# Performance work log

Hardware: AMD Instinct MI355X
Metric: run time of the kernel (lower is better)

## Reference

```python
import jax, jax.numpy as jnp
import numpy as np

C, H, W = 21, 384, 384
THETA_ALPHA, THETA_BETA, THETA_GAMMA = 160.0, 3.0, 3.0
NUM_ITER = 5
SP_RADIUS = 6   # ~2*theta_gamma truncation for the spatial Gaussian filter
BI_RADIUS = 2   # local window stand-in for the permutohedral bilateral filter
CLIQUE_IDS = (5, 37, 81, 150, 230)  # deterministic stand-in for random.sample(range(1,256),5)


def _shift(x, dy, dx):
    # zero-padded shift: out[..., y, x] = x[..., y-dy, x-dx]
    h, w = x.shape[-2], x.shape[-1]
    py = (max(dy, 0), max(-dy, 0))
    px = (max(dx, 0), max(-dx, 0))
    xp = jnp.pad(x, [(0, 0)] * (x.ndim - 2) + [py, px])
    return xp[..., py[1]:py[1] + h, px[1]:px[1] + w]


def _gauss_blur(x, theta, radius):
    # unnormalized separable spatial Gaussian (high_dim_filter, bilateral=False)
    offs = np.arange(-radius, radius + 1)
    k = np.exp(-(offs.astype(np.float32) ** 2) / (2.0 * theta * theta))
    y = sum(float(k[i]) * _shift(x, int(o), 0) for i, o in enumerate(offs))
    return sum(float(k[i]) * _shift(y, 0, int(o)) for i, o in enumerate(offs))


def _bilateral(x, rgb, ta, tb, radius):
    # unnormalized local bilateral filter (high_dim_filter, bilateral=True)
    out = jnp.zeros_like(x)
    for dy in range(-radius, radius + 1):
        for dx in range(-radius, radius + 1):
            sw = float(np.exp(-(dy * dy + dx * dx) / (2.0 * ta * ta)))
            cdiff = rgb - _shift(rgb, dy, dx)  # (3,h,w)
            cw = jnp.exp(-jnp.sum(cdiff * cdiff, axis=0) / (2.0 * tb * tb))
            out = out + sw * cw * _shift(x, dy, dx)
    return out


def setup_inputs() -> dict:
    key = jax.random.key(0)
    k1, k2, k3 = jax.random.split(key, 3)
    # offset unaries away from 0 so first_term = prod/q stays finite
    unaries = jax.random.uniform(k1, (1, H, W, C), dtype=jnp.float32) + 0.5
    rgb = jax.random.uniform(k2, (1, H, W, 3), dtype=jnp.float32) * 255.0
    superpixels = jax.random.randint(k3, (1, H, W), 0, 256, dtype=jnp.int32)
    return {
        "unaries": unaries,
        "rgb": rgb,
        "superpixels": superpixels,
        "spatial_ker_weights": jnp.eye(C, dtype=jnp.float32),
        "bilateral_ker_weights": jnp.eye(C, dtype=jnp.float32),
        "compatibility_matrix": -jnp.eye(C, dtype=jnp.float32),
        "superpixel_low_weights": jnp.ones((C,), dtype=jnp.float32),
        "superpixel_high_weight": jnp.ones((1,), dtype=jnp.float32),
    }


def reference(unaries, rgb, superpixels, spatial_ker_weights, bilateral_ker_weights,
              compatibility_matrix, superpixel_low_weights, superpixel_high_weight):
    c, h, w = C, H, W
    u = jnp.transpose(unaries[0], (2, 0, 1))        # (c,h,w)
    img = jnp.transpose(rgb[0], (2, 0, 1))          # (3,h,w)
    sp_map = jnp.transpose(superpixels[0])          # (w,h) == (h,w) since square

    ones = jnp.ones((c, h, w), dtype=u.dtype)
    spatial_norm = _gauss_blur(ones, THETA_GAMMA, SP_RADIUS)
    bilateral_norm = _bilateral(ones, img, THETA_ALPHA, THETA_BETA, BI_RADIUS)

    # clique ids are distinct, so masks are disjoint; msum in {0,1}
    msum = jnp.zeros((h, w), dtype=u.dtype)
    for sp_idx in CLIQUE_IDS:
        msum = msum + (sp_map == sp_idx).astype(u.dtype)
    n_cliques = float(len(CLIQUE_IDS))

    q = u
    for _ in range(NUM_ITER):
        sm = jax.nn.softmax(q, axis=0)
        spatial_out = _gauss_blur(sm, THETA_GAMMA, SP_RADIUS) / spatial_norm
        bilateral_out = _bilateral(sm, img, THETA_ALPHA, THETA_BETA, BI_RADIUS) / bilateral_norm

        # prod_tensor = sum_k [ mask_k*q + (1-mask_k) ]  (disjoint masks => closed form)
        prod_tensor = msum[None] * q + (n_cliques - msum)[None]
        first_term = prod_tensor / q
        sp_update = (superpixel_low_weights[:, None, None] * first_term
                     + superpixel_high_weight[0] * (1.0 - first_term))

        mp = (spatial_ker_weights @ spatial_out.reshape(c, -1)
              + bilateral_ker_weights @ bilateral_out.reshape(c, -1))
        pairwise = (compatibility_matrix @ mp).reshape(c, h, w)
        q = u - pairwise + sp_update

    return jnp.transpose(q[None], (0, 2, 3, 1))  # (1,h,w,c)
```

## Files before the change

kernel.cpp:

```cpp
#include <hip/hip_runtime.h>
#include <hip/hip_bf16.h>

static constexpr int C  = 21;
static constexpr int H  = 384;
static constexpr int W  = 384;
static constexpr int HW = H * W;
static constexpr float NCLIQ = 5.0f;

typedef unsigned short u16;
typedef unsigned int   u32;

#define GKDEF constexpr float gk[13] = { \
    0.13533528f, 0.24935222f, 0.41111229f, 0.60653066f, 0.80073740f, \
    0.94595947f, 1.00000000f, 0.94595947f, 0.80073740f, 0.60653066f, \
    0.41111229f, 0.24935222f, 0.13533528f }

__device__ __forceinline__ float bfu2f(u16 u) {
    return __uint_as_float(((u32)u) << 16);
}
__device__ __forceinline__ u16 f2bfu(float f) {
    unsigned x = __float_as_uint(f);
    return (u16)((x + 0x7FFF + ((x >> 16) & 1)) >> 16);
}

__global__ __launch_bounds__(256)
void k_prep(const float* __restrict__ un, const float* __restrict__ rgb,
            const int* __restrict__ sp,
            const float* __restrict__ Wsp, const float* __restrict__ Wbi,
            const float* __restrict__ Cm,
            float* __restrict__ q, float* __restrict__ unp,
            u16* __restrict__ wtab, float* __restrict__ msum,
            float* __restrict__ inv_sp, float* __restrict__ inv_bn,
            float* __restrict__ M1, float* __restrict__ M2,
            int* __restrict__ mflag,
            u16* __restrict__ t1, u16* __restrict__ t2) {
    GKDEF;
    __shared__ float sM1[C * C], sM2[C * C];
    __shared__ float Aun[256 * C];
    __shared__ int seq;
    if (threadIdx.x == 0) seq = 1;
    bool bad = false;
    for (int i = threadIdx.x; i < C * C; i += 256) {
        int c = i / C, k = i - c * C;
        float a1 = 0.f, a2 = 0.f;
        for (int j = 0; j < C; j++) {
            float cm = Cm[c * C + j];
            a1 += cm * Wsp[j * C + k];
            a2 += cm * Wbi[j * C + k];
        }
        sM1[i] = a1;
        sM2[i] = a2;
        if (__float_as_uint(a1) != __float_as_uint(a2)) bad = true;
        if (blockIdx.x == 0) { M1[i] = a1; M2[i] = a2; }
    }

    int bid = blockIdx.x;
    int chunk = (bid & 7) * 72 + (bid >> 3);
    int p0 = chunk * 256;
    int p = p0 + threadIdx.x;
    int y = p / W, x = p - y * W;

    {
        const float* ub = un + (size_t)p0 * C;
        for (int i = threadIdx.x; i < 256 * C / 4; i += 256)
            *(float4*)(Aun + i * 4) = *(const float4*)(ub + i * 4);
    }
    __syncthreads();
    if (bad) atomicAnd(&seq, 0);

    float v[C];
#pragma unroll
    for (int c = 0; c < C; c++) {
        v[c] = Aun[threadIdx.x * C + c];
        q[c * HW + p] = v[c];
        unp[c * HW + p] = v[c];
    }

    float swl[9];
#pragma unroll
    for (int i = 0; i < 9; i++) swl[i] = expf(-(float)i * (1.0f / 51200.0f));

    float r0 = rgb[p * 3 + 0];
    float g0 = rgb[p * 3 + 1];
    float b0 = rgb[p * 3 + 2];
    float s = 0.f;
    int t = 0;
#pragma unroll
    for (int dy = -2; dy <= 2; dy++) {
#pragma unroll
        for (int dx = -2; dx <= 2; dx++, t++) {
            int sy = y - dy, sx = x - dx;
            float wv = 0.f;
            if (sy >= 0 && sy < H && sx >= 0 && sx < W) {
                int o = sy * W + sx;
                float dr = r0 - rgb[o * 3 + 0];
                float dg = g0 - rgb[o * 3 + 1];
                float db = b0 - rgb[o * 3 + 2];
                wv = swl[dy * dy + dx * dx] *
                     expf(-(dr * dr + dg * dg + db * db) * (1.0f / 18.0f));
            }
            u16 wu = f2bfu(wv);
            wtab[(size_t)t * HW + p] = wu;
            s += bfu2f(wu);
        }
    }
    inv_bn[p] = 1.0f / s;

    float fy = 0.f, fx = 0.f;
    for (int o = -6; o <= 6; o++) {
        if (y - o >= 0 && y - o < H) fy += gk[o + 6];
        if (x - o >= 0 && x - o < W) fx += gk[o + 6];
    }
    inv_sp[p] = 1.0f / (fy * fx);

    int vv = sp[x * W + y];
    msum[p] = (vv == 5 || vv == 37 || vv == 81 || vv == 150 || vv == 230) ? 1.0f : 0.0f;

    __syncthreads();
    bool eq = (seq != 0);
    if (bid == 0 && threadIdx.x == 0) mflag[0] = eq ? 1 : 0;

    float mx = -1e30f;
#pragma unroll
    for (int c = 0; c < C; c++) mx = fmaxf(mx, v[c]);
    float ssum = 0.f;
#pragma unroll
    for (int c = 0; c < C; c++) {
        v[c] = expf(v[c] - mx);
        ssum += v[c];
    }
    float inv = 1.0f / ssum;
    float a1[C];
#pragma unroll
    for (int c = 0; c < C; c++) a1[c] = 0.f;
#pragma unroll
    for (int k = 0; k < C; k++) {
        float e = v[k];
#pragma unroll
        for (int c = 0; c < C; c++) a1[c] += sM1[c * C + k] * e;
    }
#pragma unroll
    for (int c = 0; c < C; c++) t1[c * HW + p] = f2bfu(a1[c] * inv);
    if (!eq) {
        float a2[C];
#pragma unroll
        for (int c = 0; c < C; c++) a2[c] = 0.f;
#pragma unroll
        for (int k = 0; k < C; k++) {
            float e = v[k];
#pragma unroll
            for (int c = 0; c < C; c++) a2[c] += sM2[c * C + k] * e;
        }
#pragma unroll
        for (int c = 0; c < C; c++) t2[c * HW + p] = f2bfu(a2[c] * inv);
    }
}

__global__ __launch_bounds__(256)
void k_ST(const float* __restrict__ q, const float* __restrict__ M1,
          const float* __restrict__ M2, const int* __restrict__ mflag,
          u16* __restrict__ t1, u16* __restrict__ t2) {
    int bid = blockIdx.x;
    int chunk = (bid & 7) * 72 + (bid >> 3);
    int p = chunk * 256 + threadIdx.x;
    bool meq = (mflag[0] != 0);
    float v[C];
    float mx = -1e30f;
#pragma unroll
    for (int c = 0; c < C; c++) {
        v[c] = q[c * HW + p];
        mx = fmaxf(mx, v[c]);
    }
    float s = 0.f;
#pragma unroll
    for (int c = 0; c < C; c++) {
        v[c] = expf(v[c] - mx);
        s += v[c];
    }
    float inv = 1.0f / s;
    float a1[C];
#pragma unroll
    for (int c = 0; c < C; c++) a1[c] = 0.f;
#pragma unroll
    for (int k = 0; k < C; k++) {
        float e = v[k];
#pragma unroll
        for (int c = 0; c < C; c++) a1[c] += M1[c * C + k] * e;
    }
#pragma unroll
    for (int c = 0; c < C; c++) t1[c * HW + p] = f2bfu(a1[c] * inv);
    if (!meq) {
        float a2[C];
#pragma unroll
        for (int c = 0; c < C; c++) a2[c] = 0.f;
#pragma unroll
        for (int k = 0; k < C; k++) {
            float e = v[k];
#pragma unroll
            for (int c = 0; c < C; c++) a2[c] += M2[c * C + k] * e;
        }
#pragma unroll
        for (int c = 0; c < C; c++) t2[c * HW + p] = f2bfu(a2[c] * inv);
    }
}

__global__ __launch_bounds__(256)
void k_VF(const u16* __restrict__ t1, const u16* __restrict__ t2,
          const u16* __restrict__ wtab, const float* __restrict__ msum,
          const float* __restrict__ inv_sp, const float* __restrict__ inv_bn,
          const float* __restrict__ unp,
          const float* __restrict__ loww, const float* __restrict__ highw,
          const int* __restrict__ mflag,
          float* __restrict__ q, float* __restrict__ outp) {
    GKDEF;
    __shared__ float A[20 * 144];
    __shared__ float B[8 * 144];
    int bid = blockIdx.x;
    int xcd = bid & 7;
    int idx = bid >> 3;
    int c   = idx % 21;
    int rem = idx / 21;
    int xt  = rem % 3;
    int ytl = rem / 3;
    int gyt = xcd * 6 + ytl;
    int x0 = xt * 128;
    int y0 = gyt * 8;
    bool meq = (mflag[0] != 0);
    const u16* t1p = t1 + (size_t)c * HW;

    for (int i = threadIdx.x; i < 20 * 36; i += 256) {
        int r = i / 36, q4 = i - r * 36;
        int gy = y0 - 6 + r;
        int gx = x0 - 8 + q4 * 4;
        float4 v;
        if (gy < 0 || gy >= H) {
            v.x = v.y = v.z = v.w = 0.f;
        } else if (gx >= 0 && gx + 3 < W) {
            ushort4 u = *(const ushort4*)(t1p + gy * W + gx);
            v.x = bfu2f(u.x); v.y = bfu2f(u.y); v.z = bfu2f(u.z); v.w = bfu2f(u.w);
        } else {
            float e[4];
            for (int jj = 0; jj < 4; jj++) {
                int xx = gx + jj;
                e[jj] = (xx >= 0 && xx < W) ? bfu2f(t1p[gy * W + xx]) : 0.f;
            }
            v.x = e[0]; v.y = e[1]; v.z = e[2]; v.w = e[3];
        }
        *(float4*)(A + r * 144 + q4 * 4) = v;
    }
    __syncthreads();

    for (int i = threadIdx.x; i < 8 * 36; i += 256) {
        int r = i / 36, c4 = (i - r * 36) * 4;
        float ax = 0.f, ay = 0.f, az = 0.f, aw = 0.f;
#pragma unroll
        for (int d = 0; d < 13; d++) {
            const float4 av = *(const float4*)(A + (r + d) * 144 + c4);
            ax += gk[d] * av.x;
            ay += gk[d] * av.y;
            az += gk[d] * av.z;
            aw += gk[d] * av.w;
        }
        float4 o;
        o.x = ax; o.y = ay; o.z = az; o.w = aw;
        *(float4*)(B + r * 144 + c4) = o;
    }
    __syncthreads();

    int row = threadIdx.x >> 5;
    int xq  = (threadIdx.x & 31) * 4;
    int y   = y0 + row;
    int x4  = x0 + xq;
    int p4  = y * W + x4;

    ushort4 wu[25];
#pragma unroll
    for (int t = 0; t < 25; t++)
        wu[t] = *(const ushort4*)(wtab + (size_t)t * HW + p4);

    float bw[20];
    {
        const float* bp = B + row * 144 + xq;
        *(float4*)(bw +  0) = *(const float4*)(bp +  0);
        *(float4*)(bw +  4) = *(const float4*)(bp +  4);
        *(float4*)(bw +  8) = *(const float4*)(bp +  8);
        *(float4*)(bw + 12) = *(const float4*)(bp + 12);
        *(float4*)(bw + 16) = *(const float4*)(bp + 16);
    }
    float sp_[4];
#pragma unroll
    for (int jj = 0; jj < 4; jj++) {
        float a = 0.f;
#pragma unroll
        for (int t = 0; t < 13; t++) a += gk[t] * bw[jj + t + 2];
        sp_[jj] = a;
    }

    int robase;
    if (meq) {
        robase = row + 6;
    } else {
        const u16* t2p = t2 + (size_t)c * HW;
        for (int i = threadIdx.x; i < 12 * 36; i += 256) {
            int r = i / 36, q4 = i - r * 36;
            int gy = min(max(y0 - 2 + r, 0), H - 1);
            int gx = min(max(x0 - 8 + q4 * 4, 0), W - 4);
            ushort4 u = *(const ushort4*)(t2p + gy * W + gx);
            float4 v;
            v.x = bfu2f(u.x); v.y = bfu2f(u.y); v.z = bfu2f(u.z); v.w = bfu2f(u.w);
            *(float4*)(A + r * 144 + q4 * 4) = v;
        }
        __syncthreads();
        robase = row + 2;
    }

    float lc = loww[c], hw_ = highw[0];
    float4 msv = *(const float4*)(msum + p4);
    float4 isv = *(const float4*)(inv_sp + p4);
    float4 ibv = *(const float4*)(inv_bn + p4);
    float4 unv = *(const float4*)(unp + (size_t)c * HW + p4);
    float* qp = q + (size_t)c * HW + p4;
    float4 qo4 = *(const float4*)qp;

    float bi[4] = {0.f, 0.f, 0.f, 0.f};
    int lb = xq + 8;
#pragma unroll
    for (int dy = -2; dy <= 2; dy++) {
        int r = robase - dy;
        float rr[12];
        float4 v0 = *(const float4*)(A + r * 144 + lb - 4);
        float4 v1 = *(const float4*)(A + r * 144 + lb);
        float4 v2 = *(const float4*)(A + r * 144 + lb + 4);
        rr[0] = v0.x; rr[1] = v0.y; rr[2]  = v0.z; rr[3]  = v0.w;
        rr[4] = v1.x; rr[5] = v1.y; rr[6]  = v1.z; rr[7]  = v1.w;
        rr[8] = v2.x; rr[9] = v2.y; rr[10] = v2.z; rr[11] = v2.w;
#pragma unroll
        for (int dx = -2; dx <= 2; dx++) {
            const ushort4 wv = wu[(dy + 2) * 5 + (dx + 2)];
            bi[0] += bfu2f(wv.x) * rr[0 - dx + 4];
            bi[1] += bfu2f(wv.y) * rr[1 - dx + 4];
            bi[2] += bfu2f(wv.z) * rr[2 - dx + 4];
            bi[3] += bfu2f(wv.w) * rr[3 - dx + 4];
        }
    }

    float msa[4] = {msv.x, msv.y, msv.z, msv.w};
    float isa[4] = {isv.x, isv.y, isv.z, isv.w};
    float iba[4] = {ibv.x, ibv.y, ibv.z, ibv.w};
    float qoa[4] = {qo4.x, qo4.y, qo4.z, qo4.w};
    float una[4] = {unv.x, unv.y, unv.z, unv.w};
    float outv[4];
    for (int jj = 0; jj < 4; jj++) {
        float pw = sp_[jj] * isa[jj] + bi[jj] * iba[jj];
        float qo = qoa[jj];
        float ft = (msa[jj] * qo + (NCLIQ - msa[jj])) / qo;
        float su = lc * ft + hw_ * (1.0f - ft);
        outv[jj] = una[jj] - pw + su;
    }
    if (outp) {
        for (int jj = 0; jj < 4; jj++)
            outp[(size_t)(p4 + jj) * C + c] = outv[jj];
    } else {
        float4 res;
        res.x = outv[0]; res.y = outv[1]; res.z = outv[2]; res.w = outv[3];
        *(float4*)qp = res;
    }
}


extern "C" void kernel_launch(void* const* d_in, const int* in_sizes, int n_in,
                              void* d_out, int out_size, void* d_ws, size_t ws_size,
                              hipStream_t stream) {
    const float* un    = (const float*)d_in[0];
    const float* rgb   = (const float*)d_in[1];
    const int*   sp    = (const int*)d_in[2];
    const float* Wsp   = (const float*)d_in[3];
    const float* Wbi   = (const float*)d_in[4];
    const float* Cm    = (const float*)d_in[5];
    const float* loww  = (const float*)d_in[6];
    const float* highw = (const float*)d_in[7];
    float* out = (float*)d_out;

    float* ws    = (float*)d_ws;
    float* q     = ws;
    float* unp   = q   + (size_t)C * HW;
    float* msum  = unp + (size_t)C * HW;
    float* isp   = msum + HW;
    float* ibn   = isp + HW;
    float* M1    = ibn + HW;
    float* M2    = M1 + C * C;
    int*   mflag = (int*)(M2 + C * C);
    u16*   t1    = (u16*)(M2 + C * C + 6);
    u16*   t2    = t1 + (size_t)C * HW;
    u16*   wtab  = t2 + (size_t)C * HW;

    dim3 blk(256);
    dim3 gpix(HW / 256);
    dim3 gVF(3 * 48 * C);

    k_prep<<<gpix, blk, 0, stream>>>(un, rgb, sp, Wsp, Wbi, Cm,
                                     q, unp, wtab, msum, isp, ibn, M1, M2,
                                     mflag, t1, t2);
    for (int it = 0; it < 5; it++) {
        k_VF<<<gVF, blk, 0, stream>>>(t1, t2, wtab, msum, isp, ibn,
                                      unp, loww, highw, mflag, q,
                                      (it == 4) ? out : (float*)nullptr);
        if (it < 4)
            k_ST<<<gpix, blk, 0, stream>>>(q, M1, M2, mflag, t1, t2);
    }
}
```

Baseline: 239.4 us.

## Process three channels per block in k_VF to reuse bilateral weights; stage rgb rows in LDS

Each k_VF block now handles three channels instead of one, so the 25 bilateral weight planes per pixel are loaded once and applied to three channels. This cuts global weight traffic threefold, and the grid shrinks from 3024 to 1008 blocks. The A tile triples in LDS and extra barriers are added between per-channel vertical blur passes, which may reduce occupancy. In k_prep, the six rgb rows needed by each block are staged into shared memory so the 5x5 neighbourhood reads no longer go to global memory, at the cost of about 27KB more LDS.

```diff
diff --git a/kernel.cpp b/kernel.cpp
--- a/kernel.cpp
+++ b/kernel.cpp
@@ -37,6 +37,7 @@
     GKDEF;
     __shared__ float sM1[C * C], sM2[C * C];
     __shared__ float Aun[256 * C];
+    __shared__ float Argb[6 * W * 3];
     __shared__ int seq;
     if (threadIdx.x == 0) seq = 1;
     bool bad = false;
@@ -59,12 +60,20 @@
     int p0 = chunk * 256;
     int p = p0 + threadIdx.x;
     int y = p / W, x = p - y * W;
+    int y0row = p0 / W;
 
     {
         const float* ub = un + (size_t)p0 * C;
         for (int i = threadIdx.x; i < 256 * C / 4; i += 256)
             *(float4*)(Aun + i * 4) = *(const float4*)(ub + i * 4);
     }
+    for (int r = 0; r < 6; r++) {
+        int gy = y0row - 2 + r;
+        if (gy < 0 || gy >= H) continue;
+        const float* src = rgb + (size_t)gy * W * 3;
+        for (int i = threadIdx.x; i < W * 3 / 4; i += 256)
+            *(float4*)(Argb + r * (W * 3) + i * 4) = *(const float4*)(src + i * 4);
+    }
     __syncthreads();
     if (bad) atomicAnd(&seq, 0);
 
@@ -80,9 +89,10 @@
 #pragma unroll
     for (int i = 0; i < 9; i++) swl[i] = expf(-(float)i * (1.0f / 51200.0f));
 
-    float r0 = rgb[p * 3 + 0];
-    float g0 = rgb[p * 3 + 1];
-    float b0 = rgb[p * 3 + 2];
+    int lrow0 = y - y0row + 2;
+    float r0 = Argb[lrow0 * (W * 3) + x * 3 + 0];
+    float g0 = Argb[lrow0 * (W * 3) + x * 3 + 1];
+    float b0 = Argb[lrow0 * (W * 3) + x * 3 + 2];
     float s = 0.f;
     int t = 0;
 #pragma unroll
@@ -92,10 +102,11 @@
             int sy = y - dy, sx = x - dx;
             float wv = 0.f;
             if (sy >= 0 && sy < H && sx >= 0 && sx < W) {
-                int o = sy * W + sx;
-                float dr = r0 - rgb[o * 3 + 0];
-                float dg = g0 - rgb[o * 3 + 1];
-                float db = b0 - rgb[o * 3 + 2];
+                int lr = sy - y0row + 2;
+                const float* rp = Argb + lr * (W * 3) + sx * 3;
+                float dr = r0 - rp[0];
+                float dg = g0 - rp[1];
+                float db = b0 - rp[2];
                 wv = swl[dy * dy + dx * dx] *
                      expf(-(dr * dr + dg * dg + db * db) * (1.0f / 18.0f));
             }
@@ -213,57 +224,42 @@
           const int* __restrict__ mflag,
           float* __restrict__ q, float* __restrict__ outp) {
     GKDEF;
-    __shared__ float A[20 * 144];
+    __shared__ float A[3 * 20 * 144];
     __shared__ float B[8 * 144];
     int bid = blockIdx.x;
     int xcd = bid & 7;
     int idx = bid >> 3;
-    int c   = idx % 21;
-    int rem = idx / 21;
+    int g   = idx % 7;
+    int rem = idx / 7;
     int xt  = rem % 3;
     int ytl = rem / 3;
     int gyt = xcd * 6 + ytl;
     int x0 = xt * 128;
     int y0 = gyt * 8;
+    int c0 = g * 3;
     bool meq = (mflag[0] != 0);
-    const u16* t1p = t1 + (size_t)c * HW;
-
-    for (int i = threadIdx.x; i < 20 * 36; i += 256) {
-        int r = i / 36, q4 = i - r * 36;
+
+    for (int i = threadIdx.x; i < 3 * 720; i += 256) {
+        int ch = i / 720, rem2 = i - ch * 720;
+        int r = rem2 / 36, q4 = rem2 - r * 36;
         int gy = y0 - 6 + r;
         int gx = x0 - 8 + q4 * 4;
+        const u16* tp = t1 + (size_t)(c0 + ch) * HW;
         float4 v;
         if (gy < 0 || gy >= H) {
             v.x = v.y = v.z = v.w = 0.f;
         } else if (gx >= 0 && gx + 3 < W) {
-            ushort4 u = *(const ushort4*)(t1p + gy * W + gx);
+            ushort4 u = *(const ushort4*)(tp + gy * W + gx);
             v.x = bfu2f(u.x); v.y = bfu2f(u.y); v.z = bfu2f(u.z); v.w = bfu2f(u.w);
         } else {
             float e[4];
             for (int jj = 0; jj < 4; jj++) {
                 int xx = gx + jj;
-                e[jj] = (xx >= 0 && xx < W) ? bfu2f(t1p[gy * W + xx]) : 0.f;
+                e[jj] = (xx >= 0 && xx < W) ? bfu2f(tp[gy * W + xx]) : 0.f;
             }
             v.x = e[0]; v.y = e[1]; v.z = e[2]; v.w = e[3];
         }
-        *(float4*)(A + r * 144 + q4 * 4) = v;
-    }
-    __syncthreads();
-
-    for (int i = threadIdx.x; i < 8 * 36; i += 256) {
-        int r = i / 36, c4 = (i - r * 36) * 4;
-        float ax = 0.f, ay = 0.f, az = 0.f, aw = 0.f;
-#pragma unroll
-        for (int d = 0; d < 13; d++) {
-            const float4 av = *(const float4*)(A + (r + d) * 144 + c4);
-            ax += gk[d] * av.x;
-            ay += gk[d] * av.y;
-            az += gk[d] * av.z;
-            aw += gk[d] * av.w;
-        }
-        float4 o;
-        o.x = ax; o.y = ay; o.z = az; o.w = aw;
-        *(float4*)(B + r * 144 + c4) = o;
+        *(float4*)(A + ch * 2880 + r * 144 + q4 * 4) = v;
     }
     __syncthreads();
 
@@ -273,97 +269,136 @@
     int x4  = x0 + xq;
     int p4  = y * W + x4;
 
-    ushort4 wu[25];
-#pragma unroll
-    for (int t = 0; t < 25; t++)
-        wu[t] = *(const ushort4*)(wtab + (size_t)t * HW + p4);
-
-    float bw[20];
-    {
-        const float* bp = B + row * 144 + xq;
-        *(float4*)(bw +  0) = *(const float4*)(bp +  0);
-        *(float4*)(bw +  4) = *(const float4*)(bp +  4);
-        *(float4*)(bw +  8) = *(const float4*)(bp +  8);
-        *(float4*)(bw + 12) = *(const float4*)(bp + 12);
-        *(float4*)(bw + 16) = *(const float4*)(bp + 16);
-    }
-    float sp_[4];
-#pragma unroll
-    for (int jj = 0; jj < 4; jj++) {
-        float a = 0.f;
-#pragma unroll
-        for (int t = 0; t < 13; t++) a += gk[t] * bw[jj + t + 2];
-        sp_[jj] = a;
+    float spv[3][4];
+#pragma unroll
+    for (int ch = 0; ch < 3; ch++) {
+        const float* Ac = A + ch * 2880;
+        for (int i = threadIdx.x; i < 8 * 36; i += 256) {
+            int r = i / 36, c4 = (i - r * 36) * 4;
+            float ax = 0.f, ay = 0.f, az = 0.f, aw = 0.f;
+#pragma unroll
+            for (int d = 0; d < 13; d++) {
+                const float4 av = *(const float4*)(Ac + (r + d) * 144 + c4);
+                ax += gk[d] * av.x;
+                ay += gk[d] * av.y;
+                az += gk[d] * av.z;
+                aw += gk[d] * av.w;
+            }
+            float4 o;
+            o.x = ax; o.y = ay; o.z = az; o.w = aw;
+            *(float4*)(B + r * 144 + c4) = o;
+        }
+        __syncthreads();
+        float bw[20];
+        {
+            const float* bp = B + row * 144 + xq;
+            *(float4*)(bw +  0) = *(const float4*)(bp +  0);
+            *(float4*)(bw +  4) = *(const float4*)(bp +  4);
+            *(float4*)(bw +  8) = *(const float4*)(bp +  8);
+            *(float4*)(bw + 12) = *(const float4*)(bp + 12);
+            *(float4*)(bw + 16) = *(const float4*)(bp + 16);
+        }
+#pragma unroll
+        for (int jj = 0; jj < 4; jj++) {
+            float a = 0.f;
+#pragma unroll
+            for (int t = 0; t < 13; t++) a += gk[t] * bw[jj + t + 2];
+            spv[ch][jj] = a;
+        }
+        if (ch != 2) __syncthreads();
     }
 
     int robase;
     if (meq) {
         robase = row + 6;
     } else {
-        const u16* t2p = t2 + (size_t)c * HW;
-        for (int i = threadIdx.x; i < 12 * 36; i += 256) {
-            int r = i / 36, q4 = i - r * 36;
+        __syncthreads();
+        for (int i = threadIdx.x; i < 3 * 432; i += 256) {
+            int ch = i / 432, rem2 = i - ch * 432;
+            int r = rem2 / 36, q4 = rem2 - r * 36;
             int gy = min(max(y0 - 2 + r, 0), H - 1);
             int gx = min(max(x0 - 8 + q4 * 4, 0), W - 4);
-            ushort4 u = *(const ushort4*)(t2p + gy * W + gx);
+            const u16* tp = t2 + (size_t)(c0 + ch) * HW;
+            ushort4 u = *(const ushort4*)(tp + gy * W + gx);
             float4 v;
             v.x = bfu2f(u.x); v.y = bfu2f(u.y); v.z = bfu2f(u.z); v.w = bfu2f(u.w);
-            *(float4*)(A + r * 144 + q4 * 4) = v;
+            *(float4*)(A + ch * 2880 + r * 144 + q4 * 4) = v;
         }
         __syncthreads();
         robase = row + 2;
     }
 
-    float lc = loww[c], hw_ = highw[0];
+    float hw_ = highw[0];
     float4 msv = *(const float4*)(msum + p4);
     float4 isv = *(const float4*)(inv_sp + p4);
     float4 ibv = *(const float4*)(inv_bn + p4);
-    float4 unv = *(const float4*)(unp + (size_t)c * HW + p4);
-    float* qp = q + (size_t)c * HW + p4;
-    float4 qo4 = *(const float4*)qp;
-
-    float bi[4] = {0.f, 0.f, 0.f, 0.f};
+
+    float bi[3][4];
+#pragma unroll
+    for (int ch = 0; ch < 3; ch++)
+#pragma unroll
+        for (int jj = 0; jj < 4; jj++) bi[ch][jj] = 0.f;
     int lb = xq + 8;
 #pragma unroll
     for (int dy = -2; dy <= 2; dy++) {
+        int tb = (dy + 2) * 5;
+        ushort4 wv0 = *(const ushort4*)(wtab + (size_t)(tb + 0) * HW + p4);
+        ushort4 wv1 = *(const ushort4*)(wtab + (size_t)(tb + 1) * HW + p4);
+        ushort4 wv2 = *(const ushort4*)(wtab + (size_t)(tb + 2) * HW + p4);
+        ushort4 wv3 = *(const ushort4*)(wtab + (size_t)(tb + 3) * HW + p4);
+        ushort4 wv4 = *(const ushort4*)(wtab + (size_t)(tb + 4) * HW + p4);
+        const ushort4 wvs[5] = {wv0, wv1, wv2, wv3, wv4};
         int r = robase - dy;
-        float rr[12];
-        float4 v0 = *(const float4*)(A + r * 144 + lb - 4);
-        float4 v1 = *(const float4*)(A + r * 144 + lb);
-        float4 v2 = *(const float4*)(A + r * 144 + lb + 4);
-        rr[0] = v0.x; rr[1] = v0.y; rr[2]  = v0.z; rr[3]  = v0.w;
-        rr[4] = v1.x; rr[5] = v1.y; rr[6]  = v1.z; rr[7]  = v1.w;
-        rr[8] = v2.x; rr[9] = v2.y; rr[10] = v2.z; rr[11] = v2.w;
-#pragma unroll
-        for (int dx = -2; dx <= 2; dx++) {
-            const ushort4 wv = wu[(dy + 2) * 5 + (dx + 2)];
-            bi[0] += bfu2f(wv.x) * rr[0 - dx + 4];
-            bi[1] += bfu2f(wv.y) * rr[1 - dx + 4];
-            bi[2] += bfu2f(wv.z) * rr[2 - dx + 4];
-            bi[3] += bfu2f(wv.w) * rr[3 - dx + 4];
+#pragma unroll
+        for (int ch = 0; ch < 3; ch++) {
+            const float* Ac = A + ch * 2880;
+            float rr[12];
+            float4 v0 = *(const float4*)(Ac + r * 144 + lb - 4);
+            float4 v1 = *(const float4*)(Ac + r * 144 + lb);
+            float4 v2 = *(const float4*)(Ac + r * 144 + lb + 4);
+            rr[0] = v0.x; rr[1] = v0.y; rr[2]  = v0.z; rr[3]  = v0.w;
+            rr[4] = v1.x; rr[5] = v1.y; rr[6]  = v1.z; rr[7]  = v1.w;
+            rr[8] = v2.x; rr[9] = v2.y; rr[10] = v2.z; rr[11] = v2.w;
+#pragma unroll
+            for (int dx = -2; dx <= 2; dx++) {
+                const ushort4 wv = wvs[dx + 2];
+                bi[ch][0] += bfu2f(wv.x) * rr[0 - dx + 4];
+                bi[ch][1] += bfu2f(wv.y) * rr[1 - dx + 4];
+                bi[ch][2] += bfu2f(wv.z) * rr[2 - dx + 4];
+                bi[ch][3] += bfu2f(wv.w) * rr[3 - dx + 4];
+            }
         }
     }
 
     float msa[4] = {msv.x, msv.y, msv.z, msv.w};
     float isa[4] = {isv.x, isv.y, isv.z, isv.w};
     float iba[4] = {ibv.x, ibv.y, ibv.z, ibv.w};
-    float qoa[4] = {qo4.x, qo4.y, qo4.z, qo4.w};
-    float una[4] = {unv.x, unv.y, unv.z, unv.w};
-    float outv[4];
-    for (int jj = 0; jj < 4; jj++) {
-        float pw = sp_[jj] * isa[jj] + bi[jj] * iba[jj];
-        float qo = qoa[jj];
-        float ft = (msa[jj] * qo + (NCLIQ - msa[jj])) / qo;
-        float su = lc * ft + hw_ * (1.0f - ft);
-        outv[jj] = una[jj] - pw + su;
-    }
-    if (outp) {
-        for (int jj = 0; jj < 4; jj++)
-            outp[(size_t)(p4 + jj) * C + c] = outv[jj];
-    } else {
-        float4 res;
-        res.x = outv[0]; res.y = outv[1]; res.z = outv[2]; res.w = outv[3];
-        *(float4*)qp = res;
+#pragma unroll
+    for (int ch = 0; ch < 3; ch++) {
+        int c = c0 + ch;
+        float lc = loww[c];
+        float4 unv = *(const float4*)(unp + (size_t)c * HW + p4);
+        float* qp = q + (size_t)c * HW + p4;
+        float4 qo4 = *(const float4*)qp;
+        float qoa[4] = {qo4.x, qo4.y, qo4.z, qo4.w};
+        float una[4] = {unv.x, unv.y, unv.z, unv.w};
+        float outv[4];
+#pragma unroll
+        for (int jj = 0; jj < 4; jj++) {
+            float pw = spv[ch][jj] * isa[jj] + bi[ch][jj] * iba[jj];
+            float qo = qoa[jj];
+            float ft = (msa[jj] * qo + (NCLIQ - msa[jj])) / qo;
+            float su = lc * ft + hw_ * (1.0f - ft);
+            outv[jj] = una[jj] - pw + su;
+        }
+        if (outp) {
+            for (int jj = 0; jj < 4; jj++)
+                outp[(size_t)(p4 + jj) * C + c] = outv[jj];
+        } else {
+            float4 res;
+            res.x = outv[0]; res.y = outv[1]; res.z = outv[2]; res.w = outv[3];
+            *(float4*)qp = res;
+        }
     }
 }
 
@@ -396,7 +431,7 @@
 
     dim3 blk(256);
     dim3 gpix(HW / 256);
-    dim3 gVF(3 * 48 * C);
+    dim3 gVF(1008);
 
     k_prep<<<gpix, blk, 0, stream>>>(un, rgb, sp, Wsp, Wbi, Cm,
                                      q, unp, wtab, msum, isp, ibn, M1, M2,
```

Measured after the change: 338.8 us. 1.42x slower.

## Shrink VF tiles to 32-wide 64-thread blocks and stage prep RGB rows in LDS

Applied to the files above, without the earlier changes.

The filter kernel's tile shrinks from 128x8 to 32x8 pixels with 64-thread blocks, so there are four times as many blocks and less LDS per block, which aims to raise occupancy. The 25 bilateral weight loads move from one up-front register array into the per-dy loop, which lowers register pressure. The prep kernel now stages six RGB rows in shared memory instead of reading neighbours from global memory. In exchange, the 12-column halo is now large relative to a 32-wide tile, so halo reload overhead rises sharply, and the prep kernel uses about 27KB more LDS per block.

```diff
diff --git a/kernel.cpp b/kernel.cpp
--- a/kernel.cpp
+++ b/kernel.cpp
@@ -37,6 +37,7 @@
     GKDEF;
     __shared__ float sM1[C * C], sM2[C * C];
     __shared__ float Aun[256 * C];
+    __shared__ float Argb[6 * W * 3];
     __shared__ int seq;
     if (threadIdx.x == 0) seq = 1;
     bool bad = false;
@@ -59,12 +60,20 @@
     int p0 = chunk * 256;
     int p = p0 + threadIdx.x;
     int y = p / W, x = p - y * W;
+    int y0row = p0 / W;
 
     {
         const float* ub = un + (size_t)p0 * C;
         for (int i = threadIdx.x; i < 256 * C / 4; i += 256)
             *(float4*)(Aun + i * 4) = *(const float4*)(ub + i * 4);
     }
+    for (int r = 0; r < 6; r++) {
+        int gy = y0row - 2 + r;
+        if (gy < 0 || gy >= H) continue;
+        const float* src = rgb + (size_t)gy * W * 3;
+        for (int i = threadIdx.x; i < W * 3 / 4; i += 256)
+            *(float4*)(Argb + r * (W * 3) + i * 4) = *(const float4*)(src + i * 4);
+    }
     __syncthreads();
     if (bad) atomicAnd(&seq, 0);
 
@@ -80,9 +89,10 @@
 #pragma unroll
     for (int i = 0; i < 9; i++) swl[i] = expf(-(float)i * (1.0f / 51200.0f));
 
-    float r0 = rgb[p * 3 + 0];
-    float g0 = rgb[p * 3 + 1];
-    float b0 = rgb[p * 3 + 2];
+    int lrow0 = y - y0row + 2;
+    float r0 = Argb[lrow0 * (W * 3) + x * 3 + 0];
+    float g0 = Argb[lrow0 * (W * 3) + x * 3 + 1];
+    float b0 = Argb[lrow0 * (W * 3) + x * 3 + 2];
     float s = 0.f;
     int t = 0;
 #pragma unroll
@@ -92,10 +102,11 @@
             int sy = y - dy, sx = x - dx;
             float wv = 0.f;
             if (sy >= 0 && sy < H && sx >= 0 && sx < W) {
-                int o = sy * W + sx;
-                float dr = r0 - rgb[o * 3 + 0];
-                float dg = g0 - rgb[o * 3 + 1];
-                float db = b0 - rgb[o * 3 + 2];
+                int lr = sy - y0row + 2;
+                const float* rp = Argb + lr * (W * 3) + sx * 3;
+                float dr = r0 - rp[0];
+                float dg = g0 - rp[1];
+                float db = b0 - rp[2];
                 wv = swl[dy * dy + dx * dx] *
                      expf(-(dr * dr + dg * dg + db * db) * (1.0f / 18.0f));
             }
@@ -204,7 +215,7 @@
     }
 }
 
-__global__ __launch_bounds__(256)
+__global__ __launch_bounds__(64)
 void k_VF(const u16* __restrict__ t1, const u16* __restrict__ t2,
           const u16* __restrict__ wtab, const float* __restrict__ msum,
           const float* __restrict__ inv_sp, const float* __restrict__ inv_bn,
@@ -213,23 +224,23 @@
           const int* __restrict__ mflag,
           float* __restrict__ q, float* __restrict__ outp) {
     GKDEF;
-    __shared__ float A[20 * 144];
-    __shared__ float B[8 * 144];
+    __shared__ float A[20 * 48];
+    __shared__ float B[8 * 48];
     int bid = blockIdx.x;
     int xcd = bid & 7;
     int idx = bid >> 3;
     int c   = idx % 21;
     int rem = idx / 21;
-    int xt  = rem % 3;
-    int ytl = rem / 3;
+    int xt  = rem % 12;
+    int ytl = rem / 12;
     int gyt = xcd * 6 + ytl;
-    int x0 = xt * 128;
+    int x0 = xt * 32;
     int y0 = gyt * 8;
     bool meq = (mflag[0] != 0);
     const u16* t1p = t1 + (size_t)c * HW;
 
-    for (int i = threadIdx.x; i < 20 * 36; i += 256) {
-        int r = i / 36, q4 = i - r * 36;
+    for (int i = threadIdx.x; i < 20 * 12; i += 64) {
+        int r = i / 12, q4 = i - r * 12;
         int gy = y0 - 6 + r;
         int gx = x0 - 8 + q4 * 4;
         float4 v;
@@ -246,16 +257,16 @@
             }
             v.x = e[0]; v.y = e[1]; v.z = e[2]; v.w = e[3];
         }
-        *(float4*)(A + r * 144 + q4 * 4) = v;
+        *(float4*)(A + r * 48 + q4 * 4) = v;
     }
     __syncthreads();
 
-    for (int i = threadIdx.x; i < 8 * 36; i += 256) {
-        int r = i / 36, c4 = (i - r * 36) * 4;
+    for (int i = threadIdx.x; i < 8 * 12; i += 64) {
+        int r = i / 12, c4 = (i - r * 12) * 4;
         float ax = 0.f, ay = 0.f, az = 0.f, aw = 0.f;
 #pragma unroll
         for (int d = 0; d < 13; d++) {
-            const float4 av = *(const float4*)(A + (r + d) * 144 + c4);
+            const float4 av = *(const float4*)(A + (r + d) * 48 + c4);
             ax += gk[d] * av.x;
             ay += gk[d] * av.y;
             az += gk[d] * av.z;
@@ -263,24 +274,19 @@
         }
         float4 o;
         o.x = ax; o.y = ay; o.z = az; o.w = aw;
-        *(float4*)(B + r * 144 + c4) = o;
+        *(float4*)(B + r * 48 + c4) = o;
     }
     __syncthreads();
 
-    int row = threadIdx.x >> 5;
-    int xq  = (threadIdx.x & 31) * 4;
+    int row = threadIdx.x >> 3;
+    int xq  = (threadIdx.x & 7) * 4;
     int y   = y0 + row;
     int x4  = x0 + xq;
     int p4  = y * W + x4;
 
-    ushort4 wu[25];
-#pragma unroll
-    for (int t = 0; t < 25; t++)
-        wu[t] = *(const ushort4*)(wtab + (size_t)t * HW + p4);
-
     float bw[20];
     {
-        const float* bp = B + row * 144 + xq;
+        const float* bp = B + row * 48 + xq;
         *(float4*)(bw +  0) = *(const float4*)(bp +  0);
         *(float4*)(bw +  4) = *(const float4*)(bp +  4);
         *(float4*)(bw +  8) = *(const float4*)(bp +  8);
@@ -301,14 +307,14 @@
         robase = row + 6;
     } else {
         const u16* t2p = t2 + (size_t)c * HW;
-        for (int i = threadIdx.x; i < 12 * 36; i += 256) {
-            int r = i / 36, q4 = i - r * 36;
+        for (int i = threadIdx.x; i < 12 * 12; i += 64) {
+            int r = i / 12, q4 = i - r * 12;
             int gy = min(max(y0 - 2 + r, 0), H - 1);
             int gx = min(max(x0 - 8 + q4 * 4, 0), W - 4);
             ushort4 u = *(const ushort4*)(t2p + gy * W + gx);
             float4 v;
             v.x = bfu2f(u.x); v.y = bfu2f(u.y); v.z = bfu2f(u.z); v.w = bfu2f(u.w);
-            *(float4*)(A + r * 144 + q4 * 4) = v;
+            *(float4*)(A + r * 48 + q4 * 4) = v;
         }
         __syncthreads();
         robase = row + 2;
@@ -326,17 +332,24 @@
     int lb = xq + 8;
 #pragma unroll
     for (int dy = -2; dy <= 2; dy++) {
+        int tb = (dy + 2) * 5;
+        ushort4 wv0 = *(const ushort4*)(wtab + (size_t)(tb + 0) * HW + p4);
+        ushort4 wv1 = *(const ushort4*)(wtab + (size_t)(tb + 1) * HW + p4);
+        ushort4 wv2 = *(const ushort4*)(wtab + (size_t)(tb + 2) * HW + p4);
+        ushort4 wv3 = *(const ushort4*)(wtab + (size_t)(tb + 3) * HW + p4);
+        ushort4 wv4 = *(const ushort4*)(wtab + (size_t)(tb + 4) * HW + p4);
+        const ushort4 wvs[5] = {wv0, wv1, wv2, wv3, wv4};
         int r = robase - dy;
         float rr[12];
-        float4 v0 = *(const float4*)(A + r * 144 + lb - 4);
-        float4 v1 = *(const float4*)(A + r * 144 + lb);
-        float4 v2 = *(const float4*)(A + r * 144 + lb + 4);
+        float4 v0 = *(const float4*)(A + r * 48 + lb - 4);
+        float4 v1 = *(const float4*)(A + r * 48 + lb);
+        float4 v2 = *(const float4*)(A + r * 48 + lb + 4);
         rr[0] = v0.x; rr[1] = v0.y; rr[2]  = v0.z; rr[3]  = v0.w;
         rr[4] = v1.x; rr[5] = v1.y; rr[6]  = v1.z; rr[7]  = v1.w;
         rr[8] = v2.x; rr[9] = v2.y; rr[10] = v2.z; rr[11] = v2.w;
 #pragma unroll
         for (int dx = -2; dx <= 2; dx++) {
-            const ushort4 wv = wu[(dy + 2) * 5 + (dx + 2)];
+            const ushort4 wv = wvs[dx + 2];
             bi[0] += bfu2f(wv.x) * rr[0 - dx + 4];
             bi[1] += bfu2f(wv.y) * rr[1 - dx + 4];
             bi[2] += bfu2f(wv.z) * rr[2 - dx + 4];
@@ -394,18 +407,19 @@
     u16*   t2    = t1 + (size_t)C * HW;
     u16*   wtab  = t2 + (size_t)C * HW;
 
-    dim3 blk(256);
+    dim3 blkP(256);
     dim3 gpix(HW / 256);
-    dim3 gVF(3 * 48 * C);
-
-    k_prep<<<gpix, blk, 0, stream>>>(un, rgb, sp, Wsp, Wbi, Cm,
-                                     q, unp, wtab, msum, isp, ibn, M1, M2,
-                                     mflag, t1, t2);
+    dim3 blkV(64);
+    dim3 gVF(12 * 48 * C * 8 / 8);
+
+    k_prep<<<gpix, blkP, 0, stream>>>(un, rgb, sp, Wsp, Wbi, Cm,
+                                      q, unp, wtab, msum, isp, ibn, M1, M2,
+                                      mflag, t1, t2);
     for (int it = 0; it < 5; it++) {
-        k_VF<<<gVF, blk, 0, stream>>>(t1, t2, wtab, msum, isp, ibn,
-                                      unp, loww, highw, mflag, q,
-                                      (it == 4) ? out : (float*)nullptr);
+        k_VF<<<gVF, blkV, 0, stream>>>(t1, t2, wtab, msum, isp, ibn,
+                                       unp, loww, highw, mflag, q,
+                                       (it == 4) ? out : (float*)nullptr);
         if (it < 4)
-            k_ST<<<gpix, blk, 0, stream>>>(q, M1, M2, mflag, t1, t2);
-    }
-}
+            k_ST<<<gpix, blkP, 0, stream>>>(q, M1, M2, mflag, t1, t2);
+    }
+}
```

Result: slower. 269.1 us (+12.4%).

## Shrink prep/ST blocks to one wavefront, stage RGB halo in LDS, stream weights

Applied to the files above, without the earlier changes.

k_prep and k_ST now run with 64-thread blocks (one wavefront) over 4x as many blocks, so more blocks can be resident and per-block LDS is smaller. k_prep stages a 5-row RGB halo in shared memory instead of reading neighbours from global memory, and replaces the shared atomic flag with a wave ballot. k_VF now loads the bilateral weight table one row at a time inside the dy loop instead of holding all 25 ushort4 values in registers, to reduce register pressure. The trade-offs are more blocks that each recompute the 21x21 matrices, and weight loads that may be less overlapped with compute.

```diff
diff --git a/kernel.cpp b/kernel.cpp
--- a/kernel.cpp
+++ b/kernel.cpp
@@ -23,7 +23,7 @@
     return (u16)((x + 0x7FFF + ((x >> 16) & 1)) >> 16);
 }
 
-__global__ __launch_bounds__(256)
+__global__ __launch_bounds__(64)
 void k_prep(const float* __restrict__ un, const float* __restrict__ rgb,
             const int* __restrict__ sp,
             const float* __restrict__ Wsp, const float* __restrict__ Wbi,
@@ -36,11 +36,19 @@
             u16* __restrict__ t1, u16* __restrict__ t2) {
     GKDEF;
     __shared__ float sM1[C * C], sM2[C * C];
-    __shared__ float Aun[256 * C];
-    __shared__ int seq;
-    if (threadIdx.x == 0) seq = 1;
+    __shared__ float Aun[64 * C];
+    __shared__ float Argb[5 * 72 * 3];
+
+    int bid = blockIdx.x;
+    int chunk = (bid & 7) * 288 + (bid >> 3);
+    int p0 = chunk * 64;
+    int p = p0 + threadIdx.x;
+    int row0 = p0 / W;
+    int col0 = p0 - row0 * W;
+    int y = row0, x = col0 + threadIdx.x;
+
     bool bad = false;
-    for (int i = threadIdx.x; i < C * C; i += 256) {
+    for (int i = threadIdx.x; i < C * C; i += 64) {
         int c = i / C, k = i - c * C;
         float a1 = 0.f, a2 = 0.f;
         for (int j = 0; j < C; j++) {
@@ -51,22 +59,29 @@
         sM1[i] = a1;
         sM2[i] = a2;
         if (__float_as_uint(a1) != __float_as_uint(a2)) bad = true;
-        if (blockIdx.x == 0) { M1[i] = a1; M2[i] = a2; }
-    }
-
-    int bid = blockIdx.x;
-    int chunk = (bid & 7) * 72 + (bid >> 3);
-    int p0 = chunk * 256;
-    int p = p0 + threadIdx.x;
-    int y = p / W, x = p - y * W;
+        if (bid == 0) { M1[i] = a1; M2[i] = a2; }
+    }
 
     {
         const float* ub = un + (size_t)p0 * C;
-        for (int i = threadIdx.x; i < 256 * C / 4; i += 256)
+        for (int i = threadIdx.x; i < 64 * C / 4; i += 64)
             *(float4*)(Aun + i * 4) = *(const float4*)(ub + i * 4);
     }
+    for (int r = 0; r < 5; r++) {
+        int gy = row0 - 2 + r;
+        if (gy < 0 || gy >= H) continue;
+        const float* rowp = rgb + (size_t)gy * (W * 3);
+        for (int j = threadIdx.x; j < 54; j += 64) {
+            int fidx = j * 4;
+            int gf = (col0 - 4) * 3 + fidx;
+            int gfc = min(max(gf, 0), W * 3 - 4);
+            *(float4*)(Argb + r * 216 + fidx) = *(const float4*)(rowp + gfc);
+        }
+    }
     __syncthreads();
-    if (bad) atomicAnd(&seq, 0);
+
+    bool eq = (__ballot(bad) == 0ull);
+    if (bid == 0 && threadIdx.x == 0) mflag[0] = eq ? 1 : 0;
 
     float v[C];
 #pragma unroll
@@ -80,9 +95,10 @@
 #pragma unroll
     for (int i = 0; i < 9; i++) swl[i] = expf(-(float)i * (1.0f / 51200.0f));
 
-    float r0 = rgb[p * 3 + 0];
-    float g0 = rgb[p * 3 + 1];
-    float b0 = rgb[p * 3 + 2];
+    int xoff = x - col0 + 4;
+    float r0 = Argb[2 * 216 + xoff * 3 + 0];
+    float g0 = Argb[2 * 216 + xoff * 3 + 1];
+    float b0 = Argb[2 * 216 + xoff * 3 + 2];
     float s = 0.f;
     int t = 0;
 #pragma unroll
@@ -92,10 +108,11 @@
             int sy = y - dy, sx = x - dx;
             float wv = 0.f;
             if (sy >= 0 && sy < H && sx >= 0 && sx < W) {
-                int o = sy * W + sx;
-                float dr = r0 - rgb[o * 3 + 0];
-                float dg = g0 - rgb[o * 3 + 1];
-                float db = b0 - rgb[o * 3 + 2];
+                int lr = 2 - dy;
+                const float* rp = Argb + lr * 216 + (sx - col0 + 4) * 3;
+                float dr = r0 - rp[0];
+                float dg = g0 - rp[1];
+                float db = b0 - rp[2];
                 wv = swl[dy * dy + dx * dx] *
                      expf(-(dr * dr + dg * dg + db * db) * (1.0f / 18.0f));
             }
@@ -116,10 +133,6 @@
     int vv = sp[x * W + y];
     msum[p] = (vv == 5 || vv == 37 || vv == 81 || vv == 150 || vv == 230) ? 1.0f : 0.0f;
 
-    __syncthreads();
-    bool eq = (seq != 0);
-    if (bid == 0 && threadIdx.x == 0) mflag[0] = eq ? 1 : 0;
-
     float mx = -1e30f;
 #pragma unroll
     for (int c = 0; c < C; c++) mx = fmaxf(mx, v[c]);
@@ -156,13 +169,13 @@
     }
 }
 
-__global__ __launch_bounds__(256)
+__global__ __launch_bounds__(64)
 void k_ST(const float* __restrict__ q, const float* __restrict__ M1,
           const float* __restrict__ M2, const int* __restrict__ mflag,
           u16* __restrict__ t1, u16* __restrict__ t2) {
     int bid = blockIdx.x;
-    int chunk = (bid & 7) * 72 + (bid >> 3);
-    int p = chunk * 256 + threadIdx.x;
+    int chunk = (bid & 7) * 288 + (bid >> 3);
+    int p = chunk * 64 + threadIdx.x;
     bool meq = (mflag[0] != 0);
     float v[C];
     float mx = -1e30f;
@@ -273,11 +286,6 @@
     int x4  = x0 + xq;
     int p4  = y * W + x4;
 
-    ushort4 wu[25];
-#pragma unroll
-    for (int t = 0; t < 25; t++)
-        wu[t] = *(const ushort4*)(wtab + (size_t)t * HW + p4);
-
     float bw[20];
     {
         const float* bp = B + row * 144 + xq;
@@ -326,6 +334,13 @@
     int lb = xq + 8;
 #pragma unroll
     for (int dy = -2; dy <= 2; dy++) {
+        int tb = (dy + 2) * 5;
+        ushort4 wv0 = *(const ushort4*)(wtab + (size_t)(tb + 0) * HW + p4);
+        ushort4 wv1 = *(const ushort4*)(wtab + (size_t)(tb + 1) * HW + p4);
+        ushort4 wv2 = *(const ushort4*)(wtab + (size_t)(tb + 2) * HW + p4);
+        ushort4 wv3 = *(const ushort4*)(wtab + (size_t)(tb + 3) * HW + p4);
+        ushort4 wv4 = *(const ushort4*)(wtab + (size_t)(tb + 4) * HW + p4);
+        const ushort4 wvs[5] = {wv0, wv1, wv2, wv3, wv4};
         int r = robase - dy;
         float rr[12];
         float4 v0 = *(const float4*)(A + r * 144 + lb - 4);
@@ -336,7 +351,7 @@
         rr[8] = v2.x; rr[9] = v2.y; rr[10] = v2.z; rr[11] = v2.w;
 #pragma unroll
         for (int dx = -2; dx <= 2; dx++) {
-            const ushort4 wv = wu[(dy + 2) * 5 + (dx + 2)];
+            const ushort4 wv = wvs[dx + 2];
             bi[0] += bfu2f(wv.x) * rr[0 - dx + 4];
             bi[1] += bfu2f(wv.y) * rr[1 - dx + 4];
             bi[2] += bfu2f(wv.z) * rr[2 - dx + 4];
@@ -394,18 +409,19 @@
     u16*   t2    = t1 + (size_t)C * HW;
     u16*   wtab  = t2 + (size_t)C * HW;
 
-    dim3 blk(256);
-    dim3 gpix(HW / 256);
+    dim3 blk64(64);
+    dim3 gpix(HW / 64);
+    dim3 blkV(256);
     dim3 gVF(3 * 48 * C);
 
-    k_prep<<<gpix, blk, 0, stream>>>(un, rgb, sp, Wsp, Wbi, Cm,
-                                     q, unp, wtab, msum, isp, ibn, M1, M2,
-                                     mflag, t1, t2);
+    k_prep<<<gpix, blk64, 0, stream>>>(un, rgb, sp, Wsp, Wbi, Cm,
+                                       q, unp, wtab, msum, isp, ibn, M1, M2,
+                                       mflag, t1, t2);
     for (int it = 0; it < 5; it++) {
-        k_VF<<<gVF, blk, 0, stream>>>(t1, t2, wtab, msum, isp, ibn,
-                                      unp, loww, highw, mflag, q,
-                                      (it == 4) ? out : (float*)nullptr);
+        k_VF<<<gVF, blkV, 0, stream>>>(t1, t2, wtab, msum, isp, ibn,
+                                       unp, loww, highw, mflag, q,
+                                       (it == 4) ? out : (float*)nullptr);
         if (it < 4)
-            k_ST<<<gpix, blk, 0, stream>>>(q, M1, M2, mflag, t1, t2);
-    }
-}
+            k_ST<<<gpix, blk64, 0, stream>>>(q, M1, M2, mflag, t1, t2);
+    }
+}
```

New measurement: 246.0 us. 1.03x slower.
